# Kernel optimization log

Measured on AMD Instinct MI355X. Metric: run time of the kernel, lower is better.

Reference implementation:

```python
import jax, jax.numpy as jnp
import numpy as np

B, P, H, D = 32, 384, 384, 512
DA, DC, DH, NUM_LABELS = 512, 512, 512, 3


def setup_inputs() -> dict:
    key = jax.random.key(0)
    ks = jax.random.split(key, 12)
    s = lambda d: 1.0 / np.sqrt(d)
    return {
        "embedded_premise": jax.random.normal(ks[0], (B, P, D), jnp.float32),
        "embedded_hypothesis": jax.random.normal(ks[1], (B, H, D), jnp.float32),
        "premise_mask": jax.random.randint(ks[2], (B, P), 0, 2, jnp.int32),
        "hypothesis_mask": jax.random.randint(ks[3], (B, H), 0, 2, jnp.int32),
        "W_attend": jax.random.normal(ks[4], (D, DA), jnp.float32) * s(D),
        "b_attend": jnp.zeros((DA,), jnp.float32),
        "W_compare": jax.random.normal(ks[5], (2 * D, DC), jnp.float32) * s(2 * D),
        "b_compare": jnp.zeros((DC,), jnp.float32),
        "W_agg1": jax.random.normal(ks[6], (2 * DC, DH), jnp.float32) * s(2 * DC),
        "b_agg1": jnp.zeros((DH,), jnp.float32),
        "W_agg2": jax.random.normal(ks[7], (DH, NUM_LABELS), jnp.float32) * s(DH),
        "b_agg2": jnp.zeros((NUM_LABELS,), jnp.float32),
    }


def masked_softmax(scores, mask):
    # AllenNLP (legacy, non-memory-efficient) masked_softmax:
    # softmax(scores * mask), re-mask, renormalize with epsilon.
    result = jax.nn.softmax(scores * mask, axis=-1)
    result = result * mask
    return result / (jnp.sum(result, axis=-1, keepdims=True) + 1e-13)


def reference(embedded_premise, embedded_hypothesis, premise_mask, hypothesis_mask,
              W_attend, b_attend, W_compare, b_compare,
              W_agg1, b_agg1, W_agg2, b_agg2):
    pm = premise_mask.astype(jnp.float32)      # [B, P]
    hm = hypothesis_mask.astype(jnp.float32)   # [B, H]

    # TimeDistributed attend feedforward (shared weights)
    proj_p = jax.nn.relu(embedded_premise @ W_attend + b_attend)      # [B, P, DA]
    proj_h = jax.nn.relu(embedded_hypothesis @ W_attend + b_attend)   # [B, H, DA]

    # Dot-product similarity matrix [B, P, H]
    sim = jnp.einsum('bpd,bhd->bph', proj_p, proj_h)

    # Cross attention with masked softmax
    p2h = masked_softmax(sim, hm[:, None, :])                          # [B, P, H]
    attended_hypothesis = jnp.einsum('bph,bhd->bpd', p2h, embedded_hypothesis)
    h2p = masked_softmax(jnp.swapaxes(sim, 1, 2), pm[:, None, :])      # [B, H, P]
    attended_premise = jnp.einsum('bhp,bpd->bhd', h2p, embedded_premise)

    # Compare feedforward on concatenated inputs, then masked sum over time
    cmp_p = jax.nn.relu(
        jnp.concatenate([embedded_premise, attended_hypothesis], axis=-1) @ W_compare + b_compare)
    compared_premise = jnp.sum(cmp_p * pm[:, :, None], axis=1)         # [B, DC]
    cmp_h = jax.nn.relu(
        jnp.concatenate([embedded_hypothesis, attended_premise], axis=-1) @ W_compare + b_compare)
    compared_hypothesis = jnp.sum(cmp_h * hm[:, :, None], axis=1)      # [B, DC]

    # Aggregate feedforward
    agg = jnp.concatenate([compared_premise, compared_hypothesis], axis=-1)
    hidden = jax.nn.relu(agg @ W_agg1 + b_agg1)
    label_logits = hidden @ W_agg2 + b_agg2                            # [B, NUM_LABELS]
    label_probs = jax.nn.softmax(label_logits, axis=-1)
    return label_logits, label_probs, h2p, p2h
```

## Files before the change

### kernel.cpp

```cpp
#include <hip/hip_runtime.h>
#include <hip/hip_bf16.h>
#include <math.h>

typedef __bf16 bf16_t;
typedef __bf16 bf16x8 __attribute__((ext_vector_type(8)));
typedef float f32x4 __attribute__((ext_vector_type(4)));

#define NPH 12288
#define SIM_B (384*384)
#define EMB_B (384*512)

#define OUT_LOGITS 0
#define OUT_PROBS 96
#define OUT_H2P 192
#define OUT_P2H (192 + 32*384*384)

#define OFF_WATH 0L
#define OFF_WATL 524288L
#define OFF_WCT  1048576L
#define OFF_A    2097152L
#define OFF_SIM  52428800L
#define OFF_CM   71303168L
#define OFF_CS   (OFF_CM + 49152L)
#define OFF_GP   (OFF_CS + 49152L)
#define OFF_H    (OFF_GP + 524288L)

#define PROJ_LO   6291456L
#define PROJ_Z    12582912L
#define ATT_ALL_E 12582912L
#define CMP_Z     6291456L

#define BM 128
#define BN 128
#define BKK 32

#define M_PROJ   0
#define M_SPLITB 1
#define M_PLAIN  2
#define M_CONCAT 3
#define O_F32   0
#define O_BF16  1
#define O_SPLIT 2

__device__ inline void gload16(const void* g, void* l) {
    __builtin_amdgcn_global_load_lds(
        (const __attribute__((address_space(1))) void*)g,
        (__attribute__((address_space(3))) void*)l, 16, 0, 0);
}

template<bool SPLIT>
__device__ inline void stage_sw(const float* __restrict__ s,
                                bf16_t* hi, bf16_t* lo, int row, int c0)
{
    float xs[16];
    *(float4*)&xs[0]  = *(const float4*)(s);
    *(float4*)&xs[4]  = *(const float4*)(s + 4);
    *(float4*)&xs[8]  = *(const float4*)(s + 8);
    *(float4*)&xs[12] = *(const float4*)(s + 12);
    bf16x8 h0, h1, l0, l1;
    #pragma unroll
    for (int i = 0; i < 8; i++) {
        float x = xs[i];     bf16_t hh = (bf16_t)x; h0[i] = hh;
        float y = xs[i + 8]; bf16_t hy = (bf16_t)y; h1[i] = hy;
        if (SPLIT) { l0[i] = (bf16_t)(x - (float)hh); l1[i] = (bf16_t)(y - (float)hy); }
    }
    const int key = (row >> 1) & 3;
    const int cc0 = c0 ^ key, cc1 = cc0 ^ 1;
    *(bf16x8*)&hi[row * 32 + cc0 * 8] = h0;
    *(bf16x8*)&hi[row * 32 + cc1 * 8] = h1;
    if (SPLIT) {
        *(bf16x8*)&lo[row * 32 + cc0 * 8] = l0;
        *(bf16x8*)&lo[row * 32 + cc1 * 8] = l1;
    }
}

template<int MODE, int OUTK, bool BIAS, bool RELU>
__global__ __launch_bounds__(256) void mgemm(
    const float* __restrict__ Af, const float* __restrict__ Af2, int zalt,
    const bf16_t* __restrict__ Abh, long loA,
    const bf16_t* __restrict__ A2b, long a2B,
    const bf16_t* __restrict__ Bbh, long loB,
    const float* __restrict__ bias,
    float* __restrict__ Cf, bf16_t* __restrict__ Cb, long loC,
    int K, int K1,
    long aB, long bB, long cB,
    int lda, int lda2, int ldb, int ldc)
{
    constexpr int NS = (MODE == M_PROJ || MODE == M_SPLITB) ? 2 : 1;
    __shared__ bf16_t As[NS][BM * BKK];
    __shared__ bf16_t Bs[NS][BM * BKK];

    const int tid = threadIdx.x;
    const long z = blockIdx.z;
    const int m0 = blockIdx.y * BM, n0 = blockIdx.x * BN;

    const float* Afs = (MODE == M_PROJ || MODE == M_PLAIN || MODE == M_CONCAT)
                       ? ((z >= zalt) ? Af2 : Af) : nullptr;

    const int sr = tid >> 1, sc = (tid & 1) * 16, c0 = (tid & 1) * 2;
    const int gr = tid >> 2;
    const int gco = ((tid & 3) ^ ((gr >> 1) & 3)) * 8;
    const int wlds = (tid >> 6) * 512;

    const int l = tid & 63;
    const int wv = tid >> 6;
    const int wr = (wv >> 1) * 64, wc = (wv & 1) * 64;
    const int fr = l & 15, fq = l >> 4;

    f32x4 acc[4][4] = {};

    for (int k0 = 0; k0 < K; k0 += BKK) {
        if (MODE == M_PROJ || MODE == M_PLAIN) {
            const float* s = Afs + z * aB + (long)(m0 + sr) * lda + k0 + sc;
            stage_sw<MODE == M_PROJ>(s, As[0], As[NS - 1], sr, c0);
        } else if (MODE == M_CONCAT) {
            if (k0 < K1) {
                const float* s = Afs + z * aB + (long)(m0 + sr) * lda + k0 + sc;
                stage_sw<false>(s, As[0], nullptr, sr, c0);
            } else {
                const bf16_t* s = A2b + z * a2B + (long)(m0 + gr) * lda2 + (k0 - K1) + gco;
                gload16(s, &As[0][wlds]);
                gload16(s + (long)64 * lda2, &As[0][2048 + wlds]);
            }
        } else {
            const bf16_t* s = Abh + z * aB + (long)(m0 + gr) * lda + k0 + gco;
            gload16(s, &As[0][wlds]);
            gload16(s + (long)64 * lda, &As[0][2048 + wlds]);
            gload16(s + loA, &As[NS - 1][wlds]);
            gload16(s + loA + (long)64 * lda, &As[NS - 1][2048 + wlds]);
        }
        {
            const bf16_t* s = Bbh + z * bB + (long)(n0 + gr) * ldb + k0 + gco;
            gload16(s, &Bs[0][wlds]);
            gload16(s + (long)64 * ldb, &Bs[0][2048 + wlds]);
            if (NS == 2) {
                gload16(s + loB, &Bs[NS - 1][wlds]);
                gload16(s + loB + (long)64 * ldb, &Bs[NS - 1][2048 + wlds]);
            }
        }
        __syncthreads();

        bf16x8 a_h[4], b_h[4], a_l[4], b_l[4];
        #pragma unroll
        for (int i = 0; i < 4; i++) {
            const int ra = wr + i * 16 + fr;
            const int rb = wc + i * 16 + fr;
            const int ka = (fq ^ ((ra >> 1) & 3)) * 8;
            const int kb = (fq ^ ((rb >> 1) & 3)) * 8;
            a_h[i] = *(const bf16x8*)&As[0][ra * 32 + ka];
            b_h[i] = *(const bf16x8*)&Bs[0][rb * 32 + kb];
            if (NS == 2) {
                a_l[i] = *(const bf16x8*)&As[NS - 1][ra * 32 + ka];
                b_l[i] = *(const bf16x8*)&Bs[NS - 1][rb * 32 + kb];
            }
        }
        #pragma unroll
        for (int mi = 0; mi < 4; mi++)
            #pragma unroll
            for (int ni = 0; ni < 4; ni++) {
                acc[mi][ni] = __builtin_amdgcn_mfma_f32_16x16x32_bf16(a_h[mi], b_h[ni], acc[mi][ni], 0, 0, 0);
                if (NS == 2) {
                    acc[mi][ni] = __builtin_amdgcn_mfma_f32_16x16x32_bf16(a_h[mi], b_l[ni], acc[mi][ni], 0, 0, 0);
                    acc[mi][ni] = __builtin_amdgcn_mfma_f32_16x16x32_bf16(a_l[mi], b_h[ni], acc[mi][ni], 0, 0, 0);
                }
            }
        __syncthreads();
    }

    #pragma unroll
    for (int ni = 0; ni < 4; ni++) {
        const int col = n0 + wc + ni * 16 + fr;
        const float bv = BIAS ? bias[col] : 0.f;
        #pragma unroll
        for (int mi = 0; mi < 4; mi++) {
            #pragma unroll
            for (int j = 0; j < 4; j++) {
                const int row = m0 + wr + mi * 16 + fq * 4 + j;
                float v = acc[mi][ni][j] + bv;
                if (RELU) v = fmaxf(v, 0.f);
                const long idx = z * cB + (long)row * ldc + col;
                if (OUTK == O_F32) Cf[idx] = v;
                else if (OUTK == O_BF16) Cb[idx] = (bf16_t)v;
                else {
                    bf16_t h = (bf16_t)v;
                    Cb[idx] = h;
                    Cb[idx + loC] = (bf16_t)(v - (float)h);
                }
            }
        }
    }
}

template<bool SPLIT>
__global__ __launch_bounds__(256) void transpose_kernel(
    const float* __restrict__ in, const float* __restrict__ in2, int zsplit,
    bf16_t* __restrict__ out, bf16_t* __restrict__ outLo,
    int R, int C, long inB, long outB)
{
    __shared__ float tile[32][33];
    const int z = blockIdx.z;
    const float* src = (z >= zsplit) ? (in2 + (long)(z - zsplit) * inB)
                                     : (in + (long)z * inB);
    const int x0 = blockIdx.x * 32, y0 = blockIdx.y * 32;
    const int tx = threadIdx.x & 31, ty = threadIdx.x >> 5;
    #pragma unroll
    for (int i = 0; i < 32; i += 8)
        tile[ty + i][tx] = src[(long)(y0 + ty + i) * C + x0 + tx];
    __syncthreads();
    bf16_t* dst = out + (long)z * outB;
    bf16_t* dstL = SPLIT ? (outLo + (long)z * outB) : nullptr;
    #pragma unroll
    for (int i = 0; i < 32; i += 8) {
        float v = tile[tx][ty + i];
        bf16_t h = (bf16_t)v;
        dst[(long)(x0 + ty + i) * R + y0 + tx] = h;
        if (SPLIT) dstL[(long)(x0 + ty + i) * R + y0 + tx] = (bf16_t)(v - (float)h);
    }
}

__global__ __launch_bounds__(384) void masked_softmax_row(
    const float* __restrict__ S, const int* __restrict__ mask,
    float* __restrict__ out)
{
    const int row = blockIdx.x;
    const int b = row / 384;
    const int t = threadIdx.x;
    __shared__ float redmax[6], redsum[6];

    float v = S[(long)row * 384 + t];
    int mm = mask[b * 384 + t];

    float x = mm ? v : -3.4e38f;
    #pragma unroll
    for (int o = 32; o > 0; o >>= 1) x = fmaxf(x, __shfl_xor(x, o, 64));
    int wid = t >> 6, lane = t & 63;
    if (lane == 0) redmax[wid] = x;
    __syncthreads();
    float mx = redmax[0];
    #pragma unroll
    for (int w = 1; w < 6; w++) mx = fmaxf(mx, redmax[w]);

    float e = mm ? expf(v - mx) : 0.f;
    float s = e;
    #pragma unroll
    for (int o = 32; o > 0; o >>= 1) s += __shfl_xor(s, o, 64);
    if (lane == 0) redsum[wid] = s;
    __syncthreads();
    float tot = 0.f;
    #pragma unroll
    for (int w = 0; w < 6; w++) tot += redsum[w];

    out[(long)row * 384 + t] = (tot > 0.f) ? e / tot : 0.f;
}

__global__ __launch_bounds__(256) void col_stats(
    const float* __restrict__ S, const int* __restrict__ mask,
    float* __restrict__ cmax, float* __restrict__ csum)
{
    __shared__ int pml[384];
    __shared__ float mred[4][64], sred[4][64];
    const int b = blockIdx.y;
    const int h0 = blockIdx.x * 64;
    const int t = threadIdx.x;
    const int tk = t >> 6, hh = t & 63;

    for (int i = t; i < 384; i += 256) pml[i] = mask[b * 384 + i];
    __syncthreads();

    const float* Sb = S + (long)b * SIM_B + h0 + hh;
    float m = -3.4e38f;
    for (int p = tk; p < 384; p += 4)
        if (pml[p]) m = fmaxf(m, Sb[(long)p * 384]);
    mred[tk][hh] = m;
    __syncthreads();
    const float M = fmaxf(fmaxf(mred[0][hh], mred[1][hh]),
                          fmaxf(mred[2][hh], mred[3][hh]));
    float s = 0.f;
    for (int p = tk; p < 384; p += 4)
        if (pml[p]) s += expf(Sb[(long)p * 384] - M);
    sred[tk][hh] = s;
    __syncthreads();
    if (t < 64) {
        const float Mf = fmaxf(fmaxf(mred[0][t], mred[1][t]),
                               fmaxf(mred[2][t], mred[3][t]));
        cmax[b * 384 + h0 + t] = Mf;
        csum[b * 384 + h0 + t] = sred[0][t] + sred[1][t] + sred[2][t] + sred[3][t];
    }
}

__global__ __launch_bounds__(256) void col_write(
    const float* __restrict__ S, const int* __restrict__ mask,
    const float* __restrict__ cmax, const float* __restrict__ csum,
    float* __restrict__ out)
{
    __shared__ float tile[32][33];
    const int b = blockIdx.z;
    const int h0 = blockIdx.x * 32, p0 = blockIdx.y * 32;
    const int tx = threadIdx.x & 31, ty = threadIdx.x >> 5;
    const float* src = S + (long)b * SIM_B;
    #pragma unroll
    for (int i = 0; i < 32; i += 8)
        tile[ty + i][tx] = src[(long)(p0 + ty + i) * 384 + h0 + tx];
    __syncthreads();
    const int pm_v = mask[b * 384 + p0 + tx];
    float* dst = out + (long)b * SIM_B;
    #pragma unroll
    for (int i = 0; i < 32; i += 8) {
        const int h = h0 + ty + i;
        const float mx = cmax[b * 384 + h];
        const float tot = csum[b * 384 + h];
        float v = tile[tx][ty + i];
        float r = (pm_v && tot > 0.f) ? expf(v - mx) / tot : 0.f;
        dst[(long)h * 384 + p0 + tx] = r;
    }
}

__global__ __launch_bounds__(128) void masked_sum_kernel(
    const bf16_t* __restrict__ cmpb, const int* __restrict__ pm,
    const int* __restrict__ hm, float* __restrict__ Gp)
{
    const int b = blockIdx.z;
    const int pc = blockIdx.y & 3, half = blockIdx.y >> 2;
    const int d = blockIdx.x * 128 + threadIdx.x;
    const int* mrow = (half ? hm : pm) + b * 384;
    const bf16_t* base = cmpb + (long)half * CMP_Z + (long)b * EMB_B + d;
    float acc = 0.f;
    const int p0 = pc * 96;
    for (int p = p0; p < p0 + 96; p++)
        acc += (float)base[(long)p * 512] * (float)mrow[p];
    Gp[((long)pc * 32 + b) * 1024 + half * 512 + d] = acc;
}

__global__ __launch_bounds__(256) void hidden_kernel(
    const float* __restrict__ Gp, const float* __restrict__ W1,
    const float* __restrict__ b1, float* __restrict__ Hbuf)
{
    __shared__ float g[1024];
    __shared__ float part[4][64];
    const int b = blockIdx.y, j0 = blockIdx.x * 64;
    const int t = threadIdx.x;
    for (int i = t; i < 1024; i += 256)
        g[i] = Gp[((long)0 * 32 + b) * 1024 + i] + Gp[((long)1 * 32 + b) * 1024 + i]
             + Gp[((long)2 * 32 + b) * 1024 + i] + Gp[((long)3 * 32 + b) * 1024 + i];
    __syncthreads();
    const int tj = t & 63, tk = t >> 6;
    const float* w = W1 + (long)(tk * 256) * 512 + j0 + tj;
    const float* gk = g + tk * 256;
    float acc = 0.f;
    #pragma unroll 8
    for (int k = 0; k < 256; k++)
        acc = fmaf(gk[k], w[(long)k * 512], acc);
    part[tk][tj] = acc;
    __syncthreads();
    if (t < 64) {
        float v = part[0][t] + part[1][t] + part[2][t] + part[3][t] + b1[j0 + t];
        Hbuf[(long)b * 512 + j0 + t] = fmaxf(v, 0.f);
    }
}

__global__ __launch_bounds__(64) void logits_kernel(
    const float* __restrict__ Hbuf, const float* __restrict__ W2,
    const float* __restrict__ b2, float* __restrict__ out)
{
    const int b = blockIdx.x, l = threadIdx.x;
    const float* h = Hbuf + (long)b * 512;
    float a0 = 0.f, a1 = 0.f, a2 = 0.f;
    #pragma unroll
    for (int k = l; k < 512; k += 64) {
        float hv = h[k];
        a0 = fmaf(hv, W2[k * 3 + 0], a0);
        a1 = fmaf(hv, W2[k * 3 + 1], a1);
        a2 = fmaf(hv, W2[k * 3 + 2], a2);
    }
    #pragma unroll
    for (int o = 32; o > 0; o >>= 1) {
        a0 += __shfl_xor(a0, o, 64);
        a1 += __shfl_xor(a1, o, 64);
        a2 += __shfl_xor(a2, o, 64);
    }
    if (l == 0) {
        float l0 = a0 + b2[0], l1 = a1 + b2[1], l2 = a2 + b2[2];
        float mx = fmaxf(l0, fmaxf(l1, l2));
        float e0 = expf(l0 - mx), e1 = expf(l1 - mx), e2 = expf(l2 - mx);
        float s = e0 + e1 + e2;
        out[OUT_LOGITS + b * 3 + 0] = l0;
        out[OUT_LOGITS + b * 3 + 1] = l1;
        out[OUT_LOGITS + b * 3 + 2] = l2;
        out[OUT_PROBS + b * 3 + 0] = e0 / s;
        out[OUT_PROBS + b * 3 + 1] = e1 / s;
        out[OUT_PROBS + b * 3 + 2] = e2 / s;
    }
}

extern "C" void kernel_launch(void* const* d_in, const int* in_sizes, int n_in,
                              void* d_out, int out_size, void* d_ws, size_t ws_size,
                              hipStream_t stream) {
    const float* emb_p = (const float*)d_in[0];
    const float* emb_h = (const float*)d_in[1];
    const int* pm = (const int*)d_in[2];
    const int* hm = (const int*)d_in[3];
    const float* Wa = (const float*)d_in[4];
    const float* ba = (const float*)d_in[5];
    const float* Wc = (const float*)d_in[6];
    const float* bc = (const float*)d_in[7];
    const float* W1 = (const float*)d_in[8];
    const float* b1 = (const float*)d_in[9];
    const float* W2 = (const float*)d_in[10];
    const float* b2 = (const float*)d_in[11];
    float* out = (float*)d_out;
    char* W = (char*)d_ws;

    bf16_t* WaTh  = (bf16_t*)(W + OFF_WATH);
    bf16_t* WaTl  = (bf16_t*)(W + OFF_WATL);
    bf16_t* WcT   = (bf16_t*)(W + OFF_WCT);
    bf16_t* A     = (bf16_t*)(W + OFF_A);
    float*  sim   = (float*)(W + OFF_SIM);
    float*  cmaxb = (float*)(W + OFF_CM);
    float*  csumb = (float*)(W + OFF_CS);
    float*  Gp    = (float*)(W + OFF_GP);
    float*  Hbuf  = (float*)(W + OFF_H);
    bf16_t* projs  = A;
    bf16_t* embT   = A;
    bf16_t* attAll = A + ATT_ALL_E;
    bf16_t* cmpAll = A;

    transpose_kernel<true><<<dim3(16, 16, 1), 256, 0, stream>>>(
        Wa, nullptr, 999, WaTh, WaTl, 512, 512, 0, 0);
    transpose_kernel<false><<<dim3(16, 32, 1), 256, 0, stream>>>(
        Wc, nullptr, 999, WcT, nullptr, 1024, 512, 0, 0);

    mgemm<M_PROJ, O_SPLIT, true, true><<<dim3(4, 96, 2), 256, 0, stream>>>(
        emb_p, emb_h, 1, nullptr, 0, nullptr, 0, WaTh, 262144L, ba,
        nullptr, projs, PROJ_LO,
        512, 0, 0L, 0L, PROJ_Z, 512, 0, 512, 512);

    mgemm<M_SPLITB, O_F32, false, false><<<dim3(3, 3, 32), 256, 0, stream>>>(
        nullptr, nullptr, 999, projs, PROJ_LO, nullptr, 0,
        projs + PROJ_Z, PROJ_LO, nullptr,
        sim, nullptr, 0,
        512, 0, (long)EMB_B, (long)EMB_B, (long)SIM_B, 512, 0, 512, 384);

    masked_softmax_row<<<NPH, 384, 0, stream>>>(sim, hm, out + OUT_P2H);
    col_stats<<<dim3(6, 32), 256, 0, stream>>>(sim, pm, cmaxb, csumb);
    col_write<<<dim3(12, 12, 32), 256, 0, stream>>>(sim, pm, cmaxb, csumb, out + OUT_H2P);

    transpose_kernel<false><<<dim3(16, 12, 64), 256, 0, stream>>>(
        emb_p, emb_h, 32, embT, nullptr, 384, 512, (long)EMB_B, (long)EMB_B);

    mgemm<M_PLAIN, O_BF16, false, false><<<dim3(4, 3, 64), 256, 0, stream>>>(
        out + OUT_H2P, nullptr, 1 << 30, nullptr, 0, nullptr, 0,
        embT, 0, nullptr,
        nullptr, attAll, 0,
        384, 0, (long)SIM_B, (long)EMB_B, (long)EMB_B, 384, 0, 384, 512);

    mgemm<M_CONCAT, O_BF16, true, true><<<dim3(4, 96, 2), 256, 0, stream>>>(
        emb_p, emb_h, 1, nullptr, 0,
        attAll + CMP_Z, -(long)CMP_Z,
        WcT, 0, bc,
        nullptr, cmpAll, 0,
        1024, 512, 0L, 0L, (long)CMP_Z, 512, 512, 1024, 512);

    masked_sum_kernel<<<dim3(4, 8, 32), 128, 0, stream>>>(cmpAll, pm, hm, Gp);

    hidden_kernel<<<dim3(8, 32), 256, 0, stream>>>(Gp, W1, b1, Hbuf);
    logits_kernel<<<32, 64, 0, stream>>>(Hbuf, W2, b2, out);
}
```

Before: 407.3 us.

## Fuse masked time-sum into compare GEMM epilogue and remap workgroup order

The compare GEMM now reduces its ReLU outputs, weighted by the premise or hypothesis mask, over the 128 rows of each tile in shared memory. It writes per-chunk partial sums straight into Gp, so the bf16 compare output is never stored and the separate masked_sum kernel is removed. The hidden kernel now adds three chunk partials instead of four. Separately, every mgemm launch remaps its flat block index with an interleave across groups of 8, likely meant to spread neighbouring tiles across XCDs. This adds extra shared memory and syncs in the epilogue and can change the cache locality of the other GEMMs.

```diff
diff --git a/kernel.cpp b/kernel.cpp
--- a/kernel.cpp
+++ b/kernel.cpp
@@ -41,6 +41,7 @@
 #define O_F32   0
 #define O_BF16  1
 #define O_SPLIT 2
+#define O_GSUM  3
 
 __device__ inline void gload16(const void* g, void* l) {
     __builtin_amdgcn_global_load_lds(
@@ -81,6 +82,7 @@
     const bf16_t* __restrict__ A2b, long a2B,
     const bf16_t* __restrict__ Bbh, long loB,
     const float* __restrict__ bias,
+    const int* __restrict__ pmask, const int* __restrict__ hmask,
     float* __restrict__ Cf, bf16_t* __restrict__ Cb, long loC,
     int K, int K1,
     long aB, long bB, long cB,
@@ -91,8 +93,17 @@
     __shared__ bf16_t Bs[NS][BM * BKK];
 
     const int tid = threadIdx.x;
-    const long z = blockIdx.z;
-    const int m0 = blockIdx.y * BM, n0 = blockIdx.x * BN;
+
+    const int gx = gridDim.x, gy = gridDim.y;
+    const int nwg = gx * gy * gridDim.z;
+    int flat = blockIdx.x + gx * (blockIdx.y + gy * blockIdx.z);
+    flat = (flat & 7) * (nwg >> 3) + (flat >> 3);
+    const int bz_ = flat / (gx * gy);
+    const int rem_ = flat - bz_ * (gx * gy);
+    const int by_ = rem_ / gx, bx_ = rem_ - by_ * gx;
+
+    const long z = bz_;
+    const int m0 = by_ * BM, n0 = bx_ * BN;
 
     const float* Afs = (MODE == M_PROJ || MODE == M_PLAIN || MODE == M_CONCAT)
                        ? ((z >= zalt) ? Af2 : Af) : nullptr;
@@ -167,24 +178,58 @@
         __syncthreads();
     }
 
-    #pragma unroll
-    for (int ni = 0; ni < 4; ni++) {
-        const int col = n0 + wc + ni * 16 + fr;
-        const float bv = BIAS ? bias[col] : 0.f;
+    if constexpr (OUTK == O_GSUM) {
+        __shared__ float red[8][128];
+        __shared__ int smask[128];
+        const int* mrow = (z >= zalt) ? hmask : pmask;
+        const int bb = m0 / 384;
+        const int brow0 = m0 - bb * 384;
+        if (tid < 128) smask[tid] = mrow[bb * 384 + brow0 + tid];
+        __syncthreads();
+        const int rid = (wv >> 1) * 4 + fq;
         #pragma unroll
-        for (int mi = 0; mi < 4; mi++) {
+        for (int ni = 0; ni < 4; ni++) {
+            const int c = wc + ni * 16 + fr;
+            const float bv = bias[n0 + c];
+            float local = 0.f;
             #pragma unroll
-            for (int j = 0; j < 4; j++) {
-                const int row = m0 + wr + mi * 16 + fq * 4 + j;
-                float v = acc[mi][ni][j] + bv;
-                if (RELU) v = fmaxf(v, 0.f);
-                const long idx = z * cB + (long)row * ldc + col;
-                if (OUTK == O_F32) Cf[idx] = v;
-                else if (OUTK == O_BF16) Cb[idx] = (bf16_t)v;
-                else {
-                    bf16_t h = (bf16_t)v;
-                    Cb[idx] = h;
-                    Cb[idx + loC] = (bf16_t)(v - (float)h);
+            for (int mi = 0; mi < 4; mi++)
+                #pragma unroll
+                for (int j = 0; j < 4; j++) {
+                    const int rloc = wr + mi * 16 + fq * 4 + j;
+                    float v = fmaxf(acc[mi][ni][j] + bv, 0.f);
+                    local += v * (float)smask[rloc];
+                }
+            red[rid][c] = local;
+        }
+        __syncthreads();
+        if (tid < 128) {
+            float s = 0.f;
+            #pragma unroll
+            for (int r = 0; r < 8; r++) s += red[r][tid];
+            const int pc = (m0 >> 7) % 3;
+            Cf[((long)pc * 32 + bb) * 1024 + z * 512 + n0 + tid] = s;
+        }
+    } else {
+        #pragma unroll
+        for (int ni = 0; ni < 4; ni++) {
+            const int col = n0 + wc + ni * 16 + fr;
+            const float bv = BIAS ? bias[col] : 0.f;
+            #pragma unroll
+            for (int mi = 0; mi < 4; mi++) {
+                #pragma unroll
+                for (int j = 0; j < 4; j++) {
+                    const int row = m0 + wr + mi * 16 + fq * 4 + j;
+                    float v = acc[mi][ni][j] + bv;
+                    if (RELU) v = fmaxf(v, 0.f);
+                    const long idx = z * cB + (long)row * ldc + col;
+                    if (OUTK == O_F32) Cf[idx] = v;
+                    else if (OUTK == O_BF16) Cb[idx] = (bf16_t)v;
+                    else {
+                        bf16_t h = (bf16_t)v;
+                        Cb[idx] = h;
+                        Cb[idx + loC] = (bf16_t)(v - (float)h);
+                    }
                 }
             }
         }
@@ -315,22 +360,6 @@
     }
 }
 
-__global__ __launch_bounds__(128) void masked_sum_kernel(
-    const bf16_t* __restrict__ cmpb, const int* __restrict__ pm,
-    const int* __restrict__ hm, float* __restrict__ Gp)
-{
-    const int b = blockIdx.z;
-    const int pc = blockIdx.y & 3, half = blockIdx.y >> 2;
-    const int d = blockIdx.x * 128 + threadIdx.x;
-    const int* mrow = (half ? hm : pm) + b * 384;
-    const bf16_t* base = cmpb + (long)half * CMP_Z + (long)b * EMB_B + d;
-    float acc = 0.f;
-    const int p0 = pc * 96;
-    for (int p = p0; p < p0 + 96; p++)
-        acc += (float)base[(long)p * 512] * (float)mrow[p];
-    Gp[((long)pc * 32 + b) * 1024 + half * 512 + d] = acc;
-}
-
 __global__ __launch_bounds__(256) void hidden_kernel(
     const float* __restrict__ Gp, const float* __restrict__ W1,
     const float* __restrict__ b1, float* __restrict__ Hbuf)
@@ -341,7 +370,7 @@
     const int t = threadIdx.x;
     for (int i = t; i < 1024; i += 256)
         g[i] = Gp[((long)0 * 32 + b) * 1024 + i] + Gp[((long)1 * 32 + b) * 1024 + i]
-             + Gp[((long)2 * 32 + b) * 1024 + i] + Gp[((long)3 * 32 + b) * 1024 + i];
+             + Gp[((long)2 * 32 + b) * 1024 + i];
     __syncthreads();
     const int tj = t & 63, tk = t >> 6;
     const float* w = W1 + (long)(tk * 256) * 512 + j0 + tj;
@@ -422,7 +451,6 @@
     bf16_t* projs  = A;
     bf16_t* embT   = A;
     bf16_t* attAll = A + ATT_ALL_E;
-    bf16_t* cmpAll = A;
 
     transpose_kernel<true><<<dim3(16, 16, 1), 256, 0, stream>>>(
         Wa, nullptr, 999, WaTh, WaTl, 512, 512, 0, 0);
@@ -431,12 +459,14 @@
 
     mgemm<M_PROJ, O_SPLIT, true, true><<<dim3(4, 96, 2), 256, 0, stream>>>(
         emb_p, emb_h, 1, nullptr, 0, nullptr, 0, WaTh, 262144L, ba,
+        nullptr, nullptr,
         nullptr, projs, PROJ_LO,
         512, 0, 0L, 0L, PROJ_Z, 512, 0, 512, 512);
 
     mgemm<M_SPLITB, O_F32, false, false><<<dim3(3, 3, 32), 256, 0, stream>>>(
         nullptr, nullptr, 999, projs, PROJ_LO, nullptr, 0,
         projs + PROJ_Z, PROJ_LO, nullptr,
+        nullptr, nullptr,
         sim, nullptr, 0,
         512, 0, (long)EMB_B, (long)EMB_B, (long)SIM_B, 512, 0, 512, 384);
 
@@ -450,17 +480,17 @@
     mgemm<M_PLAIN, O_BF16, false, false><<<dim3(4, 3, 64), 256, 0, stream>>>(
         out + OUT_H2P, nullptr, 1 << 30, nullptr, 0, nullptr, 0,
         embT, 0, nullptr,
+        nullptr, nullptr,
         nullptr, attAll, 0,
         384, 0, (long)SIM_B, (long)EMB_B, (long)EMB_B, 384, 0, 384, 512);
 
-    mgemm<M_CONCAT, O_BF16, true, true><<<dim3(4, 96, 2), 256, 0, stream>>>(
+    mgemm<M_CONCAT, O_GSUM, true, true><<<dim3(4, 96, 2), 256, 0, stream>>>(
         emb_p, emb_h, 1, nullptr, 0,
         attAll + CMP_Z, -(long)CMP_Z,
         WcT, 0, bc,
-        nullptr, cmpAll, 0,
-        1024, 512, 0L, 0L, (long)CMP_Z, 512, 512, 1024, 512);
-
-    masked_sum_kernel<<<dim3(4, 8, 32), 128, 0, stream>>>(cmpAll, pm, hm, Gp);
+        pm, hm,
+        Gp, nullptr, 0,
+        1024, 512, 0L, 0L, 0L, 512, 512, 1024, 512);
 
     hidden_kernel<<<dim3(8, 32), 256, 0, stream>>>(Gp, W1, b1, Hbuf);
     logits_kernel<<<32, 64, 0, stream>>>(Hbuf, W2, b2, out);
```

Measured after the change: 380.9 us. 1.07x faster.
